# Optimization experiments

Hardware: AMD Instinct MI355X
Metric: run time of the kernel (lower is better)

Reference implementation:

```python
import jax, jax.numpy as jnp
import numpy as np

WS = 7   # window size
NH = 6   # num heads

def layer_norm(x, g, b, eps=1e-5):
    m = x.mean(-1, keepdims=True)
    v = ((x - m) ** 2).mean(-1, keepdims=True)
    return (x - m) / jnp.sqrt(v + eps) * g + b

def rel_pos_index(ws):
    coords = np.stack(np.meshgrid(np.arange(ws), np.arange(ws), indexing='ij')).reshape(2, -1)
    rel = (coords[:, :, None] - coords[:, None, :]).transpose(1, 2, 0)
    rel[:, :, 0] += ws - 1
    rel[:, :, 1] += ws - 1
    rel[:, :, 0] *= 2 * ws - 1
    return rel.sum(-1)  # (ws*ws, ws*ws) numpy int

RPI = rel_pos_index(WS)

def window_partition(x, ws):
    B, H, W, C = x.shape
    return x.reshape(B, H // ws, ws, W // ws, ws, C).transpose(0, 1, 3, 2, 4, 5).reshape(-1, ws * ws, C)

def window_reverse(w, ws, B, H, W):
    return w.reshape(B, H // ws, W // ws, ws, ws, -1).transpose(0, 1, 3, 2, 4, 5).reshape(B, H, W, -1)

def make_attn_mask(H, W, ws, shift):
    # Swin shifted-window mask (constant, computed in numpy)
    img = np.zeros((1, H, W, 1), np.float32)
    cnt = 0
    for h in (slice(0, -ws), slice(-ws, -shift), slice(-shift, None)):
        for w in (slice(0, -ws), slice(-ws, -shift), slice(-shift, None)):
            img[:, h, w, :] = cnt
            cnt += 1
    mw = img.reshape(1, H // ws, ws, W // ws, ws, 1).transpose(0, 1, 3, 2, 4, 5).reshape(-1, ws * ws)
    m = mw[:, None, :] - mw[:, :, None]
    return jnp.asarray(np.where(m != 0, -100.0, 0.0).astype(np.float32))  # (nW, N, N)

def conv2d(x, w, b, padding):
    y = jax.lax.conv_general_dilated(x, w, (1, 1), padding, dimension_numbers=('NCHW', 'OIHW', 'NCHW'))
    return y + b[None, :, None, None]

def swin_block(x, H, W, shift, n1g, n1b, qkvw, qkvb, projw, projb, rel, n2g, n2b, f1w, f1b, f2w, f2b):
    B, L, C = x.shape
    hd = C // NH
    shortcut = x
    x = layer_norm(x, n1g, n1b).reshape(B, H, W, C)
    if shift > 0:
        x = jnp.roll(x, (-shift, -shift), axis=(1, 2))
    xw = window_partition(x, WS)            # (B*nW, N, C)
    nWB, N, _ = xw.shape
    qkv = (xw @ qkvw.T + qkvb).reshape(nWB, N, 3, NH, hd).transpose(2, 0, 3, 1, 4)
    q, k, v = qkv[0] * (hd ** -0.5), qkv[1], qkv[2]
    attn = jnp.einsum('whnd,whmd->whnm', q, k)
    attn = attn + rel[RPI].transpose(2, 0, 1)[None]   # relative position bias (NH,N,N)
    if shift > 0:
        mask = make_attn_mask(H, W, WS, shift)        # (nW, N, N)
        nW = mask.shape[0]
        attn = (attn.reshape(B, nW, NH, N, N) + mask[None, :, None]).reshape(nWB, NH, N, N)
    attn = jax.nn.softmax(attn, axis=-1)
    xw = jnp.einsum('whnm,whmd->wnhd', attn, v).reshape(nWB, N, C)
    xw = xw @ projw.T + projb
    x = window_reverse(xw, WS, B, H, W)
    if shift > 0:
        x = jnp.roll(x, (shift, shift), axis=(1, 2))
    x = shortcut + x.reshape(B, L, C)
    h = layer_norm(x, n2g, n2b)
    h = jax.nn.gelu(h @ f1w.T + f1b, approximate=False) @ f2w.T + f2b
    return x + h

def setup_inputs() -> dict:
    key = jax.random.key(0)
    ks = iter(jax.random.split(key, 32))
    B, C, H, W = 8, 192, 56, 56
    C2, hid = C // 2, 4 * (C // 2)
    rn = lambda shape, s=0.02: jax.random.normal(next(ks), shape, jnp.float32) * s
    return dict(
        x=jax.random.normal(next(ks), (B, C, H, W), jnp.float32),
        up_w=rn((C2, C, 3, 3)), up_b=jnp.zeros((C2,), jnp.float32),
        bn_g=jnp.ones((C2,), jnp.float32), bn_b=jnp.zeros((C2,), jnp.float32),
        bn_mean=jnp.zeros((C2,), jnp.float32), bn_var=jnp.ones((C2,), jnp.float32),
        n1g=jnp.ones((2, C2), jnp.float32), n1b=jnp.zeros((2, C2), jnp.float32),
        qkv_w=rn((2, 3 * C2, C2)), qkv_b=jnp.zeros((2, 3 * C2), jnp.float32),
        proj_w=rn((2, C2, C2)), proj_b=jnp.zeros((2, C2), jnp.float32),
        rel=rn((2, (2 * WS - 1) ** 2, NH)),
        n2g=jnp.ones((2, C2), jnp.float32), n2b=jnp.zeros((2, C2), jnp.float32),
        f1w=rn((2, hid, C2)), f1b=jnp.zeros((2, hid), jnp.float32),
        f2w=rn((2, C2, hid)), f2b=jnp.zeros((2, C2), jnp.float32),
        out_w=rn((C // 4, C2, 1, 1)), out_b=jnp.zeros((C // 4,), jnp.float32),
    )

def reference(x, up_w, up_b, bn_g, bn_b, bn_mean, bn_var, n1g, n1b, qkv_w, qkv_b, proj_w, proj_b, rel, n2g, n2b, f1w, f1b, f2w, f2b, out_w, out_b):
    B, C, H, W = x.shape
    x = jnp.repeat(jnp.repeat(x, 2, axis=2), 2, axis=3)
    x = conv2d(x, up_w, up_b, 'SAME')
    x = (x - bn_mean[None, :, None, None]) * (bn_g / jnp.sqrt(bn_var + 1e-5))[None, :, None, None] + bn_b[None, :, None, None]
    x = jax.nn.relu(x)
    H2, W2, C2 = 2 * H, 2 * W, C // 2
    t = x.reshape(B, C2, H2 * W2).transpose(0, 2, 1)   # (B, L, C2)
    for i, shift in enumerate((0, WS // 2)):
        t = swin_block(t, H2, W2, shift, n1g[i], n1b[i], qkv_w[i], qkv_b[i], proj_w[i], proj_b[i], rel[i], n2g[i], n2b[i], f1w[i], f1b[i], f2w[i], f2b[i])
    x = t.transpose(0, 2, 1).reshape(B, C2, H2, W2)
    return jax.nn.relu(conv2d(x, out_w, out_b, 'VALID'))
```

## Files before the change

### kernel.cpp

```cpp
#include <hip/hip_runtime.h>
#include <math.h>

#define M_TOK 100352
#define NHEAD 6

typedef unsigned short u16;
typedef __attribute__((ext_vector_type(8))) short bf16x8;
typedef __attribute__((ext_vector_type(4))) float f32x4;
typedef __attribute__((ext_vector_type(4))) unsigned int u32x4;

__device__ inline float bf2f(u16 u) {
    union { float f; unsigned int i; } v; v.i = ((unsigned int)u) << 16; return v.f;
}
__device__ inline u16 f2bf(float f) {
    union { float f; unsigned int i; } v; v.f = f;
    unsigned int r = v.i + 0x7fffu + ((v.i >> 16) & 1u);
    return (u16)(r >> 16);
}

__global__ __launch_bounds__(256) void cast_w_kernel(const float* __restrict__ qkvw,
        const float* __restrict__ projw, const float* __restrict__ f1w,
        const float* __restrict__ f2w, const float* __restrict__ outw,
        u16* __restrict__ Wh) {
    int i = blockIdx.x * 256 + threadIdx.x;
    if (i < 55296) Wh[i] = f2bf(qkvw[i]);
    else if (i < 73728) Wh[i] = f2bf(projw[i - 55296]);
    else if (i < 147456) Wh[i] = f2bf(f1w[i - 73728]);
    else if (i < 221184) Wh[i] = f2bf(f2w[i - 147456]);
    else if (i < 225792) Wh[i] = f2bf(outw[i - 221184]);
}

__global__ __launch_bounds__(256) void fold_kernel(const float* __restrict__ up_w,
                                                   u16* __restrict__ Wc) {
    int idx = blockIdx.x * 256 + threadIdx.x;
    if (idx >= 96 * 4 * 192) return;
    int c2 = idx / 768;
    int rem = idx - c2 * 768;
    int p = rem / 192;
    int ci = rem - p * 192;
    int po = p >> 1, pw = p & 1;
    const float* w = up_w + (c2 * 192 + ci) * 9;
    float w9[9];
#pragma unroll
    for (int k = 0; k < 9; k++) w9[k] = w[k];
    float r0[3], r1[3];
#pragma unroll
    for (int kw = 0; kw < 3; kw++) {
        if (po == 0) { r0[kw] = w9[kw];              r1[kw] = w9[3 + kw] + w9[6 + kw]; }
        else         { r0[kw] = w9[kw] + w9[3 + kw]; r1[kw] = w9[6 + kw]; }
    }
    float o00, o01, o10, o11;
    if (pw == 0) { o00 = r0[0];         o01 = r0[1] + r0[2]; o10 = r1[0];         o11 = r1[1] + r1[2]; }
    else         { o00 = r0[0] + r0[1]; o01 = r0[2];         o10 = r1[0] + r1[1]; o11 = r1[2]; }
    size_t base = ((size_t)p * 4 * 96 + c2) * 192 + ci;
    Wc[base + 0 * 96 * 192] = f2bf(o00);
    Wc[base + 1 * 96 * 192] = f2bf(o01);
    Wc[base + 2 * 96 * 192] = f2bf(o10);
    Wc[base + 3 * 96 * 192] = f2bf(o11);
}

__global__ __launch_bounds__(256) void bias_gen(const float* __restrict__ rel,
                                                float* __restrict__ BT) {
    int blkid = blockIdx.x;
    int blk = blkid / 24;
    int rem = blkid - blk * 24;
    int type = rem / 6, head = rem - (rem / 6) * 6;
    const float* relp = rel + blk * 1014;
    bool shift = (blk == 1);
    for (int i = threadIdx.x; i < 4096; i += 256) {
        int a = i >> 6, k = i & 63;
        float v;
        if (k >= 49) v = -1e30f;
        else if (a >= 49) v = 0.f;
        else {
            int ah = (a * 37) >> 8, aw = a - ah * 7;
            int kh = (k * 37) >> 8, kw = k - kh * 7;
            v = relp[((ah - kh + 6) * 13 + (aw - kw + 6)) * 6 + head];
            if (shift) {
                int lha = (type & 2) ? (ah < 4 ? 1 : 2) : 0;
                int lwa = (type & 1) ? (aw < 4 ? 1 : 2) : 0;
                int lhk = (type & 2) ? (kh < 4 ? 1 : 2) : 0;
                int lwk = (type & 1) ? (kw < 4 ? 1 : 2) : 0;
                if (lha != lhk || lwa != lwk) v -= 100.f;
            }
        }
        BT[(size_t)blkid * 4096 + i] = v;
    }
}

__global__ __launch_bounds__(256) void transpose_kernel(const float* __restrict__ x,
                                                        u16* __restrict__ xT) {
    __shared__ unsigned int ts[64 * 96];
    int b = blockIdx.y;
    int pix0 = blockIdx.x * 64;
    int tid = threadIdx.x;
    int p = tid & 63, dg = tid >> 6;
    const float* xb = x + (size_t)b * 192 * 3136 + pix0 + p;
    for (int d = dg; d < 96; d += 4) {
        float v0 = xb[(size_t)(2 * d) * 3136];
        float v1 = xb[(size_t)(2 * d + 1) * 3136];
        unsigned int pk = ((unsigned int)f2bf(v1) << 16) | (unsigned int)f2bf(v0);
        ts[p * 96 + ((d & ~31) | ((d & 31) ^ (p & 31)))] = pk;
    }
    __syncthreads();
    for (int i = tid; i < 1536; i += 256) {
        int pp = i / 24, c = i - pp * 24;
        unsigned int r[4];
#pragma unroll
        for (int j = 0; j < 4; j++) {
            int d = c * 4 + j;
            r[j] = ts[pp * 96 + ((d & ~31) | ((d & 31) ^ (pp & 31)))];
        }
        u32x4 v = {r[0], r[1], r[2], r[3]};
        *(u32x4*)&xT[((size_t)b * 3136 + pix0 + pp) * 192 + c * 8] = v;
    }
}

__global__ __launch_bounds__(256) void conv_mfma(const u16* __restrict__ xT,
        const u16* __restrict__ Wc, const float* __restrict__ up_b,
        const float* __restrict__ bn_g, const float* __restrict__ bn_b,
        const float* __restrict__ bn_m, const float* __restrict__ bn_v,
        float* __restrict__ T) {
    __shared__ u16 xs[81 * 200];
    __shared__ u16 ws[96 * 104];
    int tile = blockIdx.x, p = blockIdx.y, b = blockIdx.z;
    int po = p >> 1, pw = p & 1;
    int a0 = (tile / 7) * 8, b0 = (tile % 7) * 8;
    int rro = a0 - 1 + po, cco = b0 - 1 + pw;
    int tid = threadIdx.x;
    int w = tid >> 6, lane = tid & 63, quad = lane >> 4, l16 = lane & 15;
    int mbase = (w & 1) * 32;
    int nt0 = (w >> 1) * 3;

    for (int i = tid; i < 1944; i += 256) {
        int pix = i / 24, c = i - pix * 24;
        int rr = pix / 9, cc = pix - rr * 9;
        int gr = rro + rr, gc = cco + cc;
        u32x4 v = {0u, 0u, 0u, 0u};
        if ((unsigned)gr < 56u && (unsigned)gc < 56u)
            v = *(const u32x4*)&xT[((size_t)b * 3136 + gr * 56 + gc) * 192 + c * 8];
        *(u32x4*)&xs[pix * 200 + c * 8] = v;
    }

    f32x4 zero = {0.f, 0.f, 0.f, 0.f};
    f32x4 acc[2][3];
#pragma unroll
    for (int mi = 0; mi < 2; mi++)
#pragma unroll
        for (int ni = 0; ni < 3; ni++) acc[mi][ni] = zero;

    int aoffp[2];
#pragma unroll
    for (int mi = 0; mi < 2; mi++) {
        int pixel = mbase + mi * 16 + l16;
        aoffp[mi] = ((pixel >> 3) * 9 + (pixel & 7)) * 200;
    }

    for (int tap = 0; tap < 4; tap++) {
        int di = tap >> 1, dj = tap & 1;
        int tsh = (di * 9 + dj) * 200;
        for (int kc = 0; kc < 2; kc++) {
            __syncthreads();
            for (int i = tid; i < 1152; i += 256) {
                int r = i / 12, c = i - r * 12;
                *(u32x4*)&ws[r * 104 + c * 8] =
                    *(const u32x4*)&Wc[(((size_t)p * 4 + tap) * 96 + r) * 192 + kc * 96 + c * 8];
            }
            __syncthreads();
#pragma unroll
            for (int kk = 0; kk < 3; kk++) {
                bf16x8 af[2], bfr[3];
#pragma unroll
                for (int mi = 0; mi < 2; mi++)
                    af[mi] = *(const bf16x8*)&xs[aoffp[mi] + tsh + kc * 96 + kk * 32 + quad * 8];
#pragma unroll
                for (int ni = 0; ni < 3; ni++)
                    bfr[ni] = *(const bf16x8*)&ws[((nt0 + ni) * 16 + l16) * 104 + kk * 32 + quad * 8];
#pragma unroll
                for (int mi = 0; mi < 2; mi++)
#pragma unroll
                    for (int ni = 0; ni < 3; ni++)
                        acc[mi][ni] = __builtin_amdgcn_mfma_f32_16x16x32_bf16(
                            af[mi], bfr[ni], acc[mi][ni], 0, 0, 0);
            }
        }
    }

#pragma unroll
    for (int ni = 0; ni < 3; ni++) {
        int c2 = (nt0 + ni) * 16 + l16;
        float sc = bn_g[c2] * rsqrtf(bn_v[c2] + 1e-5f);
        float sh = (up_b[c2] - bn_m[c2]) * sc + bn_b[c2];
#pragma unroll
        for (int mi = 0; mi < 2; mi++) {
#pragma unroll
            for (int reg = 0; reg < 4; reg++) {
                int pixel = mbase + mi * 16 + quad * 4 + reg;
                int pr = pixel >> 3, pc = pixel & 7;
                int oh = 2 * (a0 + pr) + po, ow = 2 * (b0 + pc) + pw;
                size_t tok = (size_t)b * 12544 + oh * 112 + ow;
                T[tok * 96 + c2] = fmaxf(acc[mi][ni][reg] * sc + sh, 0.f);
            }
        }
    }
}

template <int EPI>
__global__ __launch_bounds__(256) void gemm_ln(const float* __restrict__ Tin,
        const u16* __restrict__ W, const float* __restrict__ g,
        const float* __restrict__ bt, const float* __restrict__ bias,
        u16* __restrict__ Cout, int N) {
    __shared__ u16 Xs[128 * 104];
    __shared__ u16 Ws[96 * 104];
    __shared__ __align__(16) float gb[192];
    int tid = threadIdx.x;
    int w = tid >> 6, lane = tid & 63, quad = lane >> 4, l16 = lane & 15;
    int mh = w & 1, nh = w >> 1;
    int n0 = blockIdx.x * 96;
    size_t m0 = (size_t)blockIdx.y * 128;

    if (tid < 192) gb[tid] = (tid < 96) ? g[tid] : bt[tid - 96];
    for (int i = tid; i < 1152; i += 256) {
        int r = i / 12, c = i - r * 12;
        *(u32x4*)&Ws[r * 104 + c * 8] = *(const u32x4*)&W[(size_t)(n0 + r) * 96 + c * 8];
    }
    __syncthreads();

    {
        int r = tid >> 1, h = tid & 1;
        const float* rowp = Tin + (m0 + r) * 96 + h * 48;
        float4 v[12];
        float s = 0.f, q = 0.f;
#pragma unroll
        for (int j = 0; j < 12; j++) {
            v[j] = *(const float4*)&rowp[j * 4];
            s += v[j].x + v[j].y + v[j].z + v[j].w;
            q += v[j].x * v[j].x + v[j].y * v[j].y + v[j].z * v[j].z + v[j].w * v[j].w;
        }
        s += __shfl_xor(s, 1, 64);
        q += __shfl_xor(q, 1, 64);
        float mean = s * (1.f / 96.f);
        float var = q * (1.f / 96.f) - mean * mean;
        float rstd = rsqrtf(var + 1e-5f);
#pragma unroll
        for (int j = 0; j < 12; j += 2) {
            float4 g0 = *(const float4*)&gb[h * 48 + j * 4];
            float4 g1 = *(const float4*)&gb[h * 48 + j * 4 + 4];
            float4 b0 = *(const float4*)&gb[96 + h * 48 + j * 4];
            float4 b1 = *(const float4*)&gb[96 + h * 48 + j * 4 + 4];
            float y0 = (v[j].x - mean) * rstd * g0.x + b0.x;
            float y1 = (v[j].y - mean) * rstd * g0.y + b0.y;
            float y2 = (v[j].z - mean) * rstd * g0.z + b0.z;
            float y3 = (v[j].w - mean) * rstd * g0.w + b0.w;
            float y4 = (v[j + 1].x - mean) * rstd * g1.x + b1.x;
            float y5 = (v[j + 1].y - mean) * rstd * g1.y + b1.y;
            float y6 = (v[j + 1].z - mean) * rstd * g1.z + b1.z;
            float y7 = (v[j + 1].w - mean) * rstd * g1.w + b1.w;
            u32x4 pk = {((unsigned int)f2bf(y1) << 16) | f2bf(y0),
                        ((unsigned int)f2bf(y3) << 16) | f2bf(y2),
                        ((unsigned int)f2bf(y5) << 16) | f2bf(y4),
                        ((unsigned int)f2bf(y7) << 16) | f2bf(y6)};
            *(u32x4*)&Xs[r * 104 + h * 48 + j * 4] = pk;
        }
    }
    __syncthreads();

    f32x4 acc[3][4];
#pragma unroll
    for (int ni = 0; ni < 3; ni++)
#pragma unroll
        for (int mi = 0; mi < 4; mi++) acc[ni][mi] = f32x4{0.f, 0.f, 0.f, 0.f};
#pragma unroll
    for (int kk = 0; kk < 3; kk++) {
        bf16x8 af[3], bf[4];
#pragma unroll
        for (int ni = 0; ni < 3; ni++)
            af[ni] = *(const bf16x8*)&Ws[(nh * 48 + ni * 16 + l16) * 104 + kk * 32 + quad * 8];
#pragma unroll
        for (int mi = 0; mi < 4; mi++)
            bf[mi] = *(const bf16x8*)&Xs[(mh * 64 + mi * 16 + l16) * 104 + kk * 32 + quad * 8];
#pragma unroll
        for (int ni = 0; ni < 3; ni++)
#pragma unroll
            for (int mi = 0; mi < 4; mi++)
                acc[ni][mi] = __builtin_amdgcn_mfma_f32_16x16x32_bf16(
                    af[ni], bf[mi], acc[ni][mi], 0, 0, 0);
    }

#pragma unroll
    for (int ni = 0; ni < 3; ni++) {
        int colb = n0 + nh * 48 + ni * 16 + quad * 4;
        float4 bv = *(const float4*)&bias[colb];
#pragma unroll
        for (int mi = 0; mi < 4; mi++) {
            size_t row = m0 + mh * 64 + mi * 16 + l16;
            float v0 = acc[ni][mi][0] + bv.x, v1 = acc[ni][mi][1] + bv.y;
            float v2 = acc[ni][mi][2] + bv.z, v3 = acc[ni][mi][3] + bv.w;
            if (EPI == 1) {
                v0 = 0.5f * v0 * (1.f + erff(v0 * 0.70710678118654752f));
                v1 = 0.5f * v1 * (1.f + erff(v1 * 0.70710678118654752f));
                v2 = 0.5f * v2 * (1.f + erff(v2 * 0.70710678118654752f));
                v3 = 0.5f * v3 * (1.f + erff(v3 * 0.70710678118654752f));
            }
            unsigned int d0 = ((unsigned int)f2bf(v1) << 16) | f2bf(v0);
            unsigned int d1 = ((unsigned int)f2bf(v3) << 16) | f2bf(v2);
            *(uint2*)&Cout[row * N + colb] = make_uint2(d0, d1);
        }
    }
}

__global__ __launch_bounds__(256) void gemm_res(const u16* __restrict__ Xh,
        const u16* __restrict__ W, const float* __restrict__ bias,
        const float* __restrict__ res, float* __restrict__ Cout, int K) {
    __shared__ u16 Xs[128 * 104];
    __shared__ u16 Ws[96 * 104];
    int tid = threadIdx.x;
    int w = tid >> 6, lane = tid & 63, quad = lane >> 4, l16 = lane & 15;
    int mh = w & 1, nh = w >> 1;
    size_t m0 = (size_t)blockIdx.x * 128;

    f32x4 acc[3][4];
#pragma unroll
    for (int ni = 0; ni < 3; ni++)
#pragma unroll
        for (int mi = 0; mi < 4; mi++) acc[ni][mi] = f32x4{0.f, 0.f, 0.f, 0.f};

    for (int k0 = 0; k0 < K; k0 += 96) {
        __syncthreads();
        for (int i = tid; i < 1536; i += 256) {
            int r = i / 12, c = i - r * 12;
            *(u32x4*)&Xs[r * 104 + c * 8] = *(const u32x4*)&Xh[(m0 + r) * K + k0 + c * 8];
        }
        for (int i = tid; i < 1152; i += 256) {
            int r = i / 12, c = i - r * 12;
            *(u32x4*)&Ws[r * 104 + c * 8] = *(const u32x4*)&W[(size_t)r * K + k0 + c * 8];
        }
        __syncthreads();
#pragma unroll
        for (int kk = 0; kk < 3; kk++) {
            bf16x8 af[3], bf[4];
#pragma unroll
            for (int ni = 0; ni < 3; ni++)
                af[ni] = *(const bf16x8*)&Ws[(nh * 48 + ni * 16 + l16) * 104 + kk * 32 + quad * 8];
#pragma unroll
            for (int mi = 0; mi < 4; mi++)
                bf[mi] = *(const bf16x8*)&Xs[(mh * 64 + mi * 16 + l16) * 104 + kk * 32 + quad * 8];
#pragma unroll
            for (int ni = 0; ni < 3; ni++)
#pragma unroll
                for (int mi = 0; mi < 4; mi++)
                    acc[ni][mi] = __builtin_amdgcn_mfma_f32_16x16x32_bf16(
                        af[ni], bf[mi], acc[ni][mi], 0, 0, 0);
        }
    }

#pragma unroll
    for (int ni = 0; ni < 3; ni++) {
        int colb = nh * 48 + ni * 16 + quad * 4;
        float4 bv = *(const float4*)&bias[colb];
#pragma unroll
        for (int mi = 0; mi < 4; mi++) {
            size_t row = m0 + mh * 64 + mi * 16 + l16;
            float4 rv = *(const float4*)&res[row * 96 + colb];
            f32x4 o = {acc[ni][mi][0] + bv.x + rv.x, acc[ni][mi][1] + bv.y + rv.y,
                       acc[ni][mi][2] + bv.z + rv.z, acc[ni][mi][3] + bv.w + rv.w};
            *(f32x4*)&Cout[row * 96 + colb] = o;
        }
    }
}

__global__ __launch_bounds__(192, 3) void attn_mfma(const u16* __restrict__ qkv,
        const float* __restrict__ BT, u16* __restrict__ ao, int shift) {
    __shared__ u16 Pl[3][64 * 72];
    __shared__ u16 vts[3][16 * 72];

    int tid = threadIdx.x;
    int w = tid >> 6, lane = tid & 63, quad = lane >> 4, l16 = lane & 15;
    int Wd = blockIdx.x;
    int bb = Wd >> 8, wl = Wd & 255, wh = wl >> 4, ww = wl & 15;
    int type = ((wh == 15) ? 2 : 0) + ((ww == 15) ? 1 : 0);

    int toks4[4], tokV;
#pragma unroll
    for (int t = 0; t < 4; t++) {
        int a = t * 16 + l16; if (a > 48) a = 48;
        int r = (a * 37) >> 8, c = a - r * 7;
        int h = wh * 7 + r, wq = ww * 7 + c;
        if (shift) { h += 3; if (h >= 112) h -= 112; wq += 3; if (wq >= 112) wq -= 112; }
        toks4[t] = bb * 12544 + h * 112 + wq;
    }
    {
        int a = lane > 48 ? 48 : lane;
        int r = (a * 37) >> 8, c = a - r * 7;
        int h = wh * 7 + r, wq = ww * 7 + c;
        if (shift) { h += 3; if (h >= 112) h -= 112; wq += 3; if (wq >= 112) wq -= 112; }
        tokV = bb * 12544 + h * 112 + wq;
    }

    u16* Pw = Pl[w];
    u16* vw = vts[w];

    for (int i = lane; i < 240; i += 64) {
        int rrow = i / 15, key = 49 + (i - rrow * 15);
        vw[rrow * 72 + key] = 0;
    }

    for (int hh = 0; hh < 2; hh++) {
        int head = w * 2 + hh;

        union { u32x4 u; bf16x8 h; } qf[4], kf[4];
#pragma unroll
        for (int t = 0; t < 4; t++) {
            u32x4 zq = {0u, 0u, 0u, 0u}, zk = {0u, 0u, 0u, 0u};
            if (quad < 2) {
                const u16* rb = qkv + (size_t)toks4[t] * 288 + head * 16 + quad * 8;
                zq = *(const u32x4*)(rb);
                zk = *(const u32x4*)(rb + 96);
            }
            qf[t].u = zq; kf[t].u = zk;
        }

        if (lane < 49) {
            const u16* vb = qkv + (size_t)tokV * 288 + head * 16 + 192;
            union { u32x4 v; unsigned int u[4]; } v0, v1;
            v0.v = *(const u32x4*)(vb);
            v1.v = *(const u32x4*)(vb + 8);
#pragma unroll
            for (int j = 0; j < 4; j++) {
                vw[(2 * j) * 72 + lane]         = (u16)(v0.u[j] & 0xffffu);
                vw[(2 * j + 1) * 72 + lane]     = (u16)(v0.u[j] >> 16);
                vw[(8 + 2 * j) * 72 + lane]     = (u16)(v1.u[j] & 0xffffu);
                vw[(8 + 2 * j + 1) * 72 + lane] = (u16)(v1.u[j] >> 16);
            }
        }

        f32x4 S[4][4];
#pragma unroll
        for (int kt = 0; kt < 4; kt++)
#pragma unroll
            for (int qt = 0; qt < 4; qt++)
                S[kt][qt] = __builtin_amdgcn_mfma_f32_16x16x32_bf16(
                    kf[kt].h, qf[qt].h, f32x4{0.f, 0.f, 0.f, 0.f}, 0, 0, 0);

        const float* bbase = BT + (size_t)(type * 6 + head) * 4096;
        float rinv[4];
#pragma unroll
        for (int qt = 0; qt < 4; qt++) {
            f32x4 bv[4];
#pragma unroll
            for (int kt = 0; kt < 4; kt++)
                bv[kt] = *(const f32x4*)&bbase[(size_t)(qt * 16 + l16) * 64 + kt * 16 + quad * 4];
            float mx = -3e38f;
#pragma unroll
            for (int kt = 0; kt < 4; kt++)
#pragma unroll
                for (int r = 0; r < 4; r++) {
                    float v = fmaf(S[kt][qt][r], 0.25f, bv[kt][r]);
                    S[kt][qt][r] = v;
                    mx = fmaxf(mx, v);
                }
            mx = fmaxf(mx, __shfl_xor(mx, 16, 64));
            mx = fmaxf(mx, __shfl_xor(mx, 32, 64));
            float sm = 0.f;
#pragma unroll
            for (int kt = 0; kt < 4; kt++)
#pragma unroll
                for (int r = 0; r < 4; r++) {
                    float e = __expf(S[kt][qt][r] - mx);
                    S[kt][qt][r] = e;
                    sm += e;
                }
            sm += __shfl_xor(sm, 16, 64);
            sm += __shfl_xor(sm, 32, 64);
            rinv[qt] = 1.0f / sm;
        }

#pragma unroll
        for (int qt = 0; qt < 4; qt++)
#pragma unroll
            for (int kt = 0; kt < 4; kt++) {
                unsigned int d0 = ((unsigned int)f2bf(S[kt][qt][1]) << 16) | f2bf(S[kt][qt][0]);
                unsigned int d1 = ((unsigned int)f2bf(S[kt][qt][3]) << 16) | f2bf(S[kt][qt][2]);
                *(uint2*)&Pw[(qt * 16 + l16) * 72 + kt * 16 + quad * 4] = make_uint2(d0, d1);
            }

        bf16x8 vf[2];
#pragma unroll
        for (int ksp = 0; ksp < 2; ksp++)
            vf[ksp] = *(const bf16x8*)&vw[l16 * 72 + ksp * 32 + quad * 8];
#pragma unroll
        for (int qt = 0; qt < 4; qt++) {
            f32x4 O = {0.f, 0.f, 0.f, 0.f};
#pragma unroll
            for (int ksp = 0; ksp < 2; ksp++) {
                bf16x8 pf = *(const bf16x8*)&Pw[(qt * 16 + l16) * 72 + ksp * 32 + quad * 8];
                O = __builtin_amdgcn_mfma_f32_16x16x32_bf16(vf[ksp], pf, O, 0, 0, 0);
            }
            int a = qt * 16 + l16;
            if (a < 49) {
                float ri = rinv[qt];
                unsigned int d0 = ((unsigned int)f2bf(O[1] * ri) << 16) | f2bf(O[0] * ri);
                unsigned int d1 = ((unsigned int)f2bf(O[3] * ri) << 16) | f2bf(O[2] * ri);
                *(uint2*)&ao[(size_t)toks4[qt] * 96 + head * 16 + quad * 4] = make_uint2(d0, d1);
            }
        }
    }
}

__global__ __launch_bounds__(256) void outconv_mfma(const float* __restrict__ T,
        const u16* __restrict__ Woc, const float* __restrict__ ob,
        float* __restrict__ out) {
    __shared__ u16 Xs[128 * 104];
    __shared__ u16 Ws[48 * 104];
    int tid = threadIdx.x;
    int w = tid >> 6, lane = tid & 63, quad = lane >> 4, l16 = lane & 15;
    int t0 = blockIdx.x * 128, b = blockIdx.y;
    size_t m0 = (size_t)b * 12544 + t0;

    for (int i = tid; i < 576; i += 256) {
        int r = i / 12, c = i - r * 12;
        *(u32x4*)&Ws[r * 104 + c * 8] = *(const u32x4*)&Woc[(size_t)r * 96 + c * 8];
    }
    {
        int r = tid >> 1, h = tid & 1;
        const float* rowp = T + (m0 + r) * 96 + h * 48;
#pragma unroll
        for (int j = 0; j < 12; j += 2) {
            float4 a = *(const float4*)&rowp[j * 4];
            float4 c2 = *(const float4*)&rowp[j * 4 + 4];
            u32x4 pk = {((unsigned int)f2bf(a.y) << 16) | f2bf(a.x),
                        ((unsigned int)f2bf(a.w) << 16) | f2bf(a.z),
                        ((unsigned int)f2bf(c2.y) << 16) | f2bf(c2.x),
                        ((unsigned int)f2bf(c2.w) << 16) | f2bf(c2.z)};
            *(u32x4*)&Xs[r * 104 + h * 48 + j * 4] = pk;
        }
    }
    __syncthreads();

    f32x4 acc[2][3];
#pragma unroll
    for (int mi = 0; mi < 2; mi++)
#pragma unroll
        for (int ni = 0; ni < 3; ni++) acc[mi][ni] = f32x4{0.f, 0.f, 0.f, 0.f};
#pragma unroll
    for (int kk = 0; kk < 3; kk++) {
        bf16x8 af[2], bfr[3];
#pragma unroll
        for (int mi = 0; mi < 2; mi++)
            af[mi] = *(const bf16x8*)&Xs[(w * 32 + mi * 16 + l16) * 104 + kk * 32 + quad * 8];
#pragma unroll
        for (int ni = 0; ni < 3; ni++)
            bfr[ni] = *(const bf16x8*)&Ws[(ni * 16 + l16) * 104 + kk * 32 + quad * 8];
#pragma unroll
        for (int mi = 0; mi < 2; mi++)
#pragma unroll
            for (int ni = 0; ni < 3; ni++)
                acc[mi][ni] = __builtin_amdgcn_mfma_f32_16x16x32_bf16(
                    af[mi], bfr[ni], acc[mi][ni], 0, 0, 0);
    }

#pragma unroll
    for (int mi = 0; mi < 2; mi++)
#pragma unroll
        for (int ni = 0; ni < 3; ni++) {
            int co = ni * 16 + l16;
            float bb = ob[co];
            f32x4 o = {fmaxf(acc[mi][ni][0] + bb, 0.f), fmaxf(acc[mi][ni][1] + bb, 0.f),
                       fmaxf(acc[mi][ni][2] + bb, 0.f), fmaxf(acc[mi][ni][3] + bb, 0.f)};
            *(f32x4*)&out[((size_t)b * 48 + co) * 12544 + t0 + w * 32 + mi * 16 + quad * 4] = o;
        }
}

extern "C" void kernel_launch(void* const* d_in, const int* in_sizes, int n_in,
                              void* d_out, int out_size, void* d_ws, size_t ws_size,
                              hipStream_t stream) {
    const float* x     = (const float*)d_in[0];
    const float* up_w  = (const float*)d_in[1];
    const float* up_b  = (const float*)d_in[2];
    const float* bn_g  = (const float*)d_in[3];
    const float* bn_b  = (const float*)d_in[4];
    const float* bn_m  = (const float*)d_in[5];
    const float* bn_v  = (const float*)d_in[6];
    const float* n1g   = (const float*)d_in[7];
    const float* n1b   = (const float*)d_in[8];
    const float* qkvw  = (const float*)d_in[9];
    const float* qkvb  = (const float*)d_in[10];
    const float* projw = (const float*)d_in[11];
    const float* projb = (const float*)d_in[12];
    const float* rel   = (const float*)d_in[13];
    const float* n2g   = (const float*)d_in[14];
    const float* n2b   = (const float*)d_in[15];
    const float* f1w   = (const float*)d_in[16];
    const float* f1b   = (const float*)d_in[17];
    const float* f2w   = (const float*)d_in[18];
    const float* f2b   = (const float*)d_in[19];
    const float* outw  = (const float*)d_in[20];
    const float* outb  = (const float*)d_in[21];
    float* out = (float*)d_out;

    char* base = (char*)d_ws;
    float* T  = (float*)base;                       base += (size_t)M_TOK * 96 * 4;
    u16* XBh  = (u16*)base;                         base += (size_t)M_TOK * 96 * 2;
    u16* BIGh = (u16*)base;                         base += (size_t)M_TOK * 384 * 2;
    u16* xT   = (u16*)base;                         base += (size_t)8 * 3136 * 192 * 2;
    u16* Wc   = (u16*)base;                         base += (size_t)16 * 96 * 192 * 2;
    u16* Wh   = (u16*)base;                         base += (size_t)225792 * 2;
    float* BT = (float*)base;
    u16* qkvwh = Wh;
    u16* projwh = Wh + 55296;
    u16* f1wh = Wh + 73728;
    u16* f2wh = Wh + 147456;
    u16* outwh = Wh + 221184;

    cast_w_kernel<<<882, 256, 0, stream>>>(qkvw, projw, f1w, f2w, outw, Wh);
    fold_kernel<<<288, 256, 0, stream>>>(up_w, Wc);
    bias_gen<<<48, 256, 0, stream>>>(rel, BT);
    transpose_kernel<<<dim3(49, 8), 256, 0, stream>>>(x, xT);
    conv_mfma<<<dim3(49, 4, 8), 256, 0, stream>>>(xT, Wc, up_b, bn_g, bn_b, bn_m, bn_v, T);

    for (int blk = 0; blk < 2; blk++) {
        int shift = (blk == 0) ? 0 : 3;
        gemm_ln<0><<<dim3(3, M_TOK / 128), 256, 0, stream>>>(
            T, qkvwh + blk * 27648, n1g + blk * 96, n1b + blk * 96, qkvb + blk * 288, BIGh, 288);
        attn_mfma<<<2048, 192, 0, stream>>>(BIGh, BT + (size_t)blk * 98304, XBh, shift);
        gemm_res<<<M_TOK / 128, 256, 0, stream>>>(
            XBh, projwh + blk * 9216, projb + blk * 96, T, T, 96);
        gemm_ln<1><<<dim3(4, M_TOK / 128), 256, 0, stream>>>(
            T, f1wh + blk * 36864, n2g + blk * 96, n2b + blk * 96, f1b + blk * 384, BIGh, 384);
        gemm_res<<<M_TOK / 128, 256, 0, stream>>>(
            BIGh, f2wh + blk * 36864, f2b + blk * 96, T, T, 384);
    }

    outconv_mfma<<<dim3(98, 8), 256, 0, stream>>>(T, outwh, outb, out);
}
```

Baseline: 636.1 us.

## Fuse LayerNorm into producer epilogues and emit bf16 activations for consumer GEMMs

LayerNorm moves out of the QKV and FC1 GEMM prologues into the epilogues of the kernels that produce their input: the up-conv, the proj residual GEMM, and the FC2 residual GEMM. The row statistics are reduced across waves through shared memory. Consumer GEMMs and the output conv now load ready-made bf16 activations instead of re-reading fp32 rows and renormalising them in every column block. This trades some extra bf16 stores and shared-memory reductions in the producers for less global traffic and less duplicated LN work. The proj GEMM reads and writes the same XBh buffer despite __restrict__, which is safe only because each block stages its own rows into shared memory before writing them.

```diff
diff --git a/kernel.cpp b/kernel.cpp
--- a/kernel.cpp
+++ b/kernel.cpp
@@ -9,9 +9,6 @@
 typedef __attribute__((ext_vector_type(4))) float f32x4;
 typedef __attribute__((ext_vector_type(4))) unsigned int u32x4;
 
-__device__ inline float bf2f(u16 u) {
-    union { float f; unsigned int i; } v; v.i = ((unsigned int)u) << 16; return v.f;
-}
 __device__ inline u16 f2bf(float f) {
     union { float f; unsigned int i; } v; v.f = f;
     unsigned int r = v.i + 0x7fffu + ((v.i >> 16) & 1u);
@@ -120,9 +117,10 @@
         const u16* __restrict__ Wc, const float* __restrict__ up_b,
         const float* __restrict__ bn_g, const float* __restrict__ bn_b,
         const float* __restrict__ bn_m, const float* __restrict__ bn_v,
-        float* __restrict__ T) {
+        const float* __restrict__ lg, const float* __restrict__ lb,
+        float* __restrict__ T, u16* __restrict__ XBh) {
     __shared__ u16 xs[81 * 200];
-    __shared__ u16 ws[96 * 104];
+    __shared__ __align__(16) u16 ws[96 * 104];
     int tile = blockIdx.x, p = blockIdx.y, b = blockIdx.z;
     int po = p >> 1, pw = p & 1;
     int a0 = (tile / 7) * 8, b0 = (tile % 7) * 8;
@@ -131,6 +129,7 @@
     int w = tid >> 6, lane = tid & 63, quad = lane >> 4, l16 = lane & 15;
     int mbase = (w & 1) * 32;
     int nt0 = (w >> 1) * 3;
+    int half = w >> 1;
 
     for (int i = tid; i < 1944; i += 256) {
         int pix = i / 24, c = i - pix * 24;
@@ -142,12 +141,11 @@
         *(u32x4*)&xs[pix * 200 + c * 8] = v;
     }
 
-    f32x4 zero = {0.f, 0.f, 0.f, 0.f};
     f32x4 acc[2][3];
 #pragma unroll
     for (int mi = 0; mi < 2; mi++)
 #pragma unroll
-        for (int ni = 0; ni < 3; ni++) acc[mi][ni] = zero;
+        for (int ni = 0; ni < 3; ni++) acc[mi][ni] = f32x4{0.f, 0.f, 0.f, 0.f};
 
     int aoffp[2];
 #pragma unroll
@@ -199,69 +197,86 @@
                 int pr = pixel >> 3, pc = pixel & 7;
                 int oh = 2 * (a0 + pr) + po, ow = 2 * (b0 + pc) + pw;
                 size_t tok = (size_t)b * 12544 + oh * 112 + ow;
-                T[tok * 96 + c2] = fmaxf(acc[mi][ni][reg] * sc + sh, 0.f);
-            }
-        }
-    }
+                float v = fmaxf(acc[mi][ni][reg] * sc + sh, 0.f);
+                acc[mi][ni][reg] = v;
+                T[tok * 96 + c2] = v;
+            }
+        }
+    }
+
+    float sA[2][4], qA[2][4];
+#pragma unroll
+    for (int mi = 0; mi < 2; mi++)
+#pragma unroll
+        for (int reg = 0; reg < 4; reg++) {
+            float s = acc[mi][0][reg] + acc[mi][1][reg] + acc[mi][2][reg];
+            float q = acc[mi][0][reg] * acc[mi][0][reg] + acc[mi][1][reg] * acc[mi][1][reg]
+                    + acc[mi][2][reg] * acc[mi][2][reg];
+#pragma unroll
+            for (int d = 1; d < 16; d <<= 1) {
+                s += __shfl_xor(s, d, 64);
+                q += __shfl_xor(q, d, 64);
+            }
+            sA[mi][reg] = s; qA[mi][reg] = q;
+        }
+    __syncthreads();
+    float2* parts = (float2*)ws;
+    if (l16 == 0) {
+#pragma unroll
+        for (int mi = 0; mi < 2; mi++)
+#pragma unroll
+            for (int reg = 0; reg < 4; reg++) {
+                int pixel = mbase + mi * 16 + quad * 4 + reg;
+                parts[pixel * 2 + half] = make_float2(sA[mi][reg], qA[mi][reg]);
+            }
+    }
+    __syncthreads();
+    float gcl[3], bcl[3];
+#pragma unroll
+    for (int ni = 0; ni < 3; ni++) {
+        int c2 = (nt0 + ni) * 16 + l16;
+        gcl[ni] = lg[c2]; bcl[ni] = lb[c2];
+    }
+#pragma unroll
+    for (int mi = 0; mi < 2; mi++)
+#pragma unroll
+        for (int reg = 0; reg < 4; reg++) {
+            int pixel = mbase + mi * 16 + quad * 4 + reg;
+            float2 oth = parts[pixel * 2 + (half ^ 1)];
+            float ts_ = sA[mi][reg] + oth.x, tq = qA[mi][reg] + oth.y;
+            float mean = ts_ * (1.f / 96.f);
+            float var = tq * (1.f / 96.f) - mean * mean;
+            float rstd = rsqrtf(var + 1e-5f);
+            int pr = pixel >> 3, pc = pixel & 7;
+            int oh = 2 * (a0 + pr) + po, ow = 2 * (b0 + pc) + pw;
+            size_t tok = (size_t)b * 12544 + oh * 112 + ow;
+#pragma unroll
+            for (int ni = 0; ni < 3; ni++) {
+                int c2 = (nt0 + ni) * 16 + l16;
+                XBh[tok * 96 + c2] = f2bf((acc[mi][ni][reg] - mean) * rstd * gcl[ni] + bcl[ni]);
+            }
+        }
 }
 
 template <int EPI>
-__global__ __launch_bounds__(256) void gemm_ln(const float* __restrict__ Tin,
-        const u16* __restrict__ W, const float* __restrict__ g,
-        const float* __restrict__ bt, const float* __restrict__ bias,
+__global__ __launch_bounds__(256) void gemm_act(const u16* __restrict__ Xh,
+        const u16* __restrict__ W, const float* __restrict__ bias,
         u16* __restrict__ Cout, int N) {
     __shared__ u16 Xs[128 * 104];
     __shared__ u16 Ws[96 * 104];
-    __shared__ __align__(16) float gb[192];
     int tid = threadIdx.x;
     int w = tid >> 6, lane = tid & 63, quad = lane >> 4, l16 = lane & 15;
     int mh = w & 1, nh = w >> 1;
     int n0 = blockIdx.x * 96;
     size_t m0 = (size_t)blockIdx.y * 128;
 
-    if (tid < 192) gb[tid] = (tid < 96) ? g[tid] : bt[tid - 96];
+    for (int i = tid; i < 1536; i += 256) {
+        int r = i / 12, c = i - r * 12;
+        *(u32x4*)&Xs[r * 104 + c * 8] = *(const u32x4*)&Xh[(m0 + r) * 96 + c * 8];
+    }
     for (int i = tid; i < 1152; i += 256) {
         int r = i / 12, c = i - r * 12;
         *(u32x4*)&Ws[r * 104 + c * 8] = *(const u32x4*)&W[(size_t)(n0 + r) * 96 + c * 8];
-    }
-    __syncthreads();
-
-    {
-        int r = tid >> 1, h = tid & 1;
-        const float* rowp = Tin + (m0 + r) * 96 + h * 48;
-        float4 v[12];
-        float s = 0.f, q = 0.f;
-#pragma unroll
-        for (int j = 0; j < 12; j++) {
-            v[j] = *(const float4*)&rowp[j * 4];
-            s += v[j].x + v[j].y + v[j].z + v[j].w;
-            q += v[j].x * v[j].x + v[j].y * v[j].y + v[j].z * v[j].z + v[j].w * v[j].w;
-        }
-        s += __shfl_xor(s, 1, 64);
-        q += __shfl_xor(q, 1, 64);
-        float mean = s * (1.f / 96.f);
-        float var = q * (1.f / 96.f) - mean * mean;
-        float rstd = rsqrtf(var + 1e-5f);
-#pragma unroll
-        for (int j = 0; j < 12; j += 2) {
-            float4 g0 = *(const float4*)&gb[h * 48 + j * 4];
-            float4 g1 = *(const float4*)&gb[h * 48 + j * 4 + 4];
-            float4 b0 = *(const float4*)&gb[96 + h * 48 + j * 4];
-            float4 b1 = *(const float4*)&gb[96 + h * 48 + j * 4 + 4];
-            float y0 = (v[j].x - mean) * rstd * g0.x + b0.x;
-            float y1 = (v[j].y - mean) * rstd * g0.y + b0.y;
-            float y2 = (v[j].z - mean) * rstd * g0.z + b0.z;
-            float y3 = (v[j].w - mean) * rstd * g0.w + b0.w;
-            float y4 = (v[j + 1].x - mean) * rstd * g1.x + b1.x;
-            float y5 = (v[j + 1].y - mean) * rstd * g1.y + b1.y;
-            float y6 = (v[j + 1].z - mean) * rstd * g1.z + b1.z;
-            float y7 = (v[j + 1].w - mean) * rstd * g1.w + b1.w;
-            u32x4 pk = {((unsigned int)f2bf(y1) << 16) | f2bf(y0),
-                        ((unsigned int)f2bf(y3) << 16) | f2bf(y2),
-                        ((unsigned int)f2bf(y5) << 16) | f2bf(y4),
-                        ((unsigned int)f2bf(y7) << 16) | f2bf(y6)};
-            *(u32x4*)&Xs[r * 104 + h * 48 + j * 4] = pk;
-        }
     }
     __syncthreads();
 
@@ -309,10 +324,13 @@
     }
 }
 
+template <int LNM>
 __global__ __launch_bounds__(256) void gemm_res(const u16* __restrict__ Xh,
         const u16* __restrict__ W, const float* __restrict__ bias,
-        const float* __restrict__ res, float* __restrict__ Cout, int K) {
-    __shared__ u16 Xs[128 * 104];
+        const float* __restrict__ res, float* __restrict__ Tout,
+        const float* __restrict__ g, const float* __restrict__ bt,
+        u16* __restrict__ Yh, int K) {
+    __shared__ __align__(16) u16 Xs[128 * 104];
     __shared__ u16 Ws[96 * 104];
     int tid = threadIdx.x;
     int w = tid >> 6, lane = tid & 63, quad = lane >> 4, l16 = lane & 15;
@@ -362,9 +380,76 @@
         for (int mi = 0; mi < 4; mi++) {
             size_t row = m0 + mh * 64 + mi * 16 + l16;
             float4 rv = *(const float4*)&res[row * 96 + colb];
-            f32x4 o = {acc[ni][mi][0] + bv.x + rv.x, acc[ni][mi][1] + bv.y + rv.y,
-                       acc[ni][mi][2] + bv.z + rv.z, acc[ni][mi][3] + bv.w + rv.w};
-            *(f32x4*)&Cout[row * 96 + colb] = o;
+            acc[ni][mi][0] += bv.x + rv.x;
+            acc[ni][mi][1] += bv.y + rv.y;
+            acc[ni][mi][2] += bv.z + rv.z;
+            acc[ni][mi][3] += bv.w + rv.w;
+            *(f32x4*)&Tout[row * 96 + colb] = acc[ni][mi];
+        }
+    }
+
+    if (LNM == 1) {
+        float sm4[4], qm4[4];
+#pragma unroll
+        for (int mi = 0; mi < 4; mi++) {
+            float s = 0.f, q = 0.f;
+#pragma unroll
+            for (int ni = 0; ni < 3; ni++)
+#pragma unroll
+                for (int r = 0; r < 4; r++) {
+                    float v = acc[ni][mi][r];
+                    s += v; q += v * v;
+                }
+            s += __shfl_xor(s, 16, 64); s += __shfl_xor(s, 32, 64);
+            q += __shfl_xor(q, 16, 64); q += __shfl_xor(q, 32, 64);
+            sm4[mi] = s; qm4[mi] = q;
+        }
+        __syncthreads();
+        float2* parts = (float2*)Xs;
+        if (quad == 0) {
+#pragma unroll
+            for (int mi = 0; mi < 4; mi++)
+                parts[(mh * 64 + mi * 16 + l16) * 2 + nh] = make_float2(sm4[mi], qm4[mi]);
+        }
+        __syncthreads();
+        float mean4[4], rstd4[4];
+#pragma unroll
+        for (int mi = 0; mi < 4; mi++) {
+            float2 oth = parts[(mh * 64 + mi * 16 + l16) * 2 + (nh ^ 1)];
+            float ts_ = sm4[mi] + oth.x, tq = qm4[mi] + oth.y;
+            float mean = ts_ * (1.f / 96.f);
+            float var = tq * (1.f / 96.f) - mean * mean;
+            mean4[mi] = mean;
+            rstd4[mi] = rsqrtf(var + 1e-5f);
+        }
+#pragma unroll
+        for (int ni = 0; ni < 3; ni++) {
+            int colb = nh * 48 + ni * 16 + quad * 4;
+            float4 g4 = *(const float4*)&g[colb];
+            float4 b4 = *(const float4*)&bt[colb];
+#pragma unroll
+            for (int mi = 0; mi < 4; mi++) {
+                size_t row = m0 + mh * 64 + mi * 16 + l16;
+                float y0 = (acc[ni][mi][0] - mean4[mi]) * rstd4[mi] * g4.x + b4.x;
+                float y1 = (acc[ni][mi][1] - mean4[mi]) * rstd4[mi] * g4.y + b4.y;
+                float y2 = (acc[ni][mi][2] - mean4[mi]) * rstd4[mi] * g4.z + b4.z;
+                float y3 = (acc[ni][mi][3] - mean4[mi]) * rstd4[mi] * g4.w + b4.w;
+                unsigned int d0 = ((unsigned int)f2bf(y1) << 16) | f2bf(y0);
+                unsigned int d1 = ((unsigned int)f2bf(y3) << 16) | f2bf(y2);
+                *(uint2*)&Yh[row * 96 + colb] = make_uint2(d0, d1);
+            }
+        }
+    } else {
+#pragma unroll
+        for (int ni = 0; ni < 3; ni++) {
+            int colb = nh * 48 + ni * 16 + quad * 4;
+#pragma unroll
+            for (int mi = 0; mi < 4; mi++) {
+                size_t row = m0 + mh * 64 + mi * 16 + l16;
+                unsigned int d0 = ((unsigned int)f2bf(acc[ni][mi][1]) << 16) | f2bf(acc[ni][mi][0]);
+                unsigned int d1 = ((unsigned int)f2bf(acc[ni][mi][3]) << 16) | f2bf(acc[ni][mi][2]);
+                *(uint2*)&Yh[row * 96 + colb] = make_uint2(d0, d1);
+            }
         }
     }
 }
@@ -507,7 +592,7 @@
     }
 }
 
-__global__ __launch_bounds__(256) void outconv_mfma(const float* __restrict__ T,
+__global__ __launch_bounds__(256) void outconv_mfma(const u16* __restrict__ Th,
         const u16* __restrict__ Woc, const float* __restrict__ ob,
         float* __restrict__ out) {
     __shared__ u16 Xs[128 * 104];
@@ -521,19 +606,9 @@
         int r = i / 12, c = i - r * 12;
         *(u32x4*)&Ws[r * 104 + c * 8] = *(const u32x4*)&Woc[(size_t)r * 96 + c * 8];
     }
-    {
-        int r = tid >> 1, h = tid & 1;
-        const float* rowp = T + (m0 + r) * 96 + h * 48;
-#pragma unroll
-        for (int j = 0; j < 12; j += 2) {
-            float4 a = *(const float4*)&rowp[j * 4];
-            float4 c2 = *(const float4*)&rowp[j * 4 + 4];
-            u32x4 pk = {((unsigned int)f2bf(a.y) << 16) | f2bf(a.x),
-                        ((unsigned int)f2bf(a.w) << 16) | f2bf(a.z),
-                        ((unsigned int)f2bf(c2.y) << 16) | f2bf(c2.x),
-                        ((unsigned int)f2bf(c2.w) << 16) | f2bf(c2.z)};
-            *(u32x4*)&Xs[r * 104 + h * 48 + j * 4] = pk;
-        }
+    for (int i = tid; i < 1536; i += 256) {
+        int r = i / 12, c = i - r * 12;
+        *(u32x4*)&Xs[r * 104 + c * 8] = *(const u32x4*)&Th[(m0 + r) * 96 + c * 8];
     }
     __syncthreads();
 
@@ -616,20 +691,29 @@
     fold_kernel<<<288, 256, 0, stream>>>(up_w, Wc);
     bias_gen<<<48, 256, 0, stream>>>(rel, BT);
     transpose_kernel<<<dim3(49, 8), 256, 0, stream>>>(x, xT);
-    conv_mfma<<<dim3(49, 4, 8), 256, 0, stream>>>(xT, Wc, up_b, bn_g, bn_b, bn_m, bn_v, T);
+    conv_mfma<<<dim3(49, 4, 8), 256, 0, stream>>>(xT, Wc, up_b, bn_g, bn_b, bn_m, bn_v,
+                                                  n1g, n1b, T, XBh);
 
     for (int blk = 0; blk < 2; blk++) {
         int shift = (blk == 0) ? 0 : 3;
-        gemm_ln<0><<<dim3(3, M_TOK / 128), 256, 0, stream>>>(
-            T, qkvwh + blk * 27648, n1g + blk * 96, n1b + blk * 96, qkvb + blk * 288, BIGh, 288);
+        gemm_act<0><<<dim3(3, M_TOK / 128), 256, 0, stream>>>(
+            XBh, qkvwh + blk * 27648, qkvb + blk * 288, BIGh, 288);
         attn_mfma<<<2048, 192, 0, stream>>>(BIGh, BT + (size_t)blk * 98304, XBh, shift);
-        gemm_res<<<M_TOK / 128, 256, 0, stream>>>(
-            XBh, projwh + blk * 9216, projb + blk * 96, T, T, 96);
-        gemm_ln<1><<<dim3(4, M_TOK / 128), 256, 0, stream>>>(
-            T, f1wh + blk * 36864, n2g + blk * 96, n2b + blk * 96, f1b + blk * 384, BIGh, 384);
-        gemm_res<<<M_TOK / 128, 256, 0, stream>>>(
-            BIGh, f2wh + blk * 36864, f2b + blk * 96, T, T, 384);
-    }
-
-    outconv_mfma<<<dim3(98, 8), 256, 0, stream>>>(T, outwh, outb, out);
-}
+        gemm_res<1><<<M_TOK / 128, 256, 0, stream>>>(
+            XBh, projwh + blk * 9216, projb + blk * 96, T, T,
+            n2g + blk * 96, n2b + blk * 96, XBh, 96);
+        gemm_act<1><<<dim3(4, M_TOK / 128), 256, 0, stream>>>(
+            XBh, f1wh + blk * 36864, f1b + blk * 384, BIGh, 384);
+        if (blk == 0) {
+            gemm_res<1><<<M_TOK / 128, 256, 0, stream>>>(
+                BIGh, f2wh + blk * 36864, f2b + blk * 96, T, T,
+                n1g + 96, n1b + 96, XBh, 384);
+        } else {
+            gemm_res<0><<<M_TOK / 128, 256, 0, stream>>>(
+                BIGh, f2wh + blk * 36864, f2b + blk * 96, T, T,
+                nullptr, nullptr, XBh, 384);
+        }
+    }
+
+    outconv_mfma<<<dim3(98, 8), 256, 0, stream>>>(XBh, outwh, outb, out);
+}
```

After: 611.5 us. 1.04x faster.
